# Optimization experiments

Measured on AMD Instinct MI355X. Metric: run time of the kernel, lower is better.

Reference implementation:

```python
import jax, jax.numpy as jnp
import numpy as np

N = 512          # data_info['n']
K = 513          # data_info['k'] + 1
B = 65536        # batch size


def _build_adjust(n, k):
    # Reproduces the __init__ mask construction exactly.
    a1 = np.ones((n - 1, k - 1, 2), dtype=np.float32)
    a2 = np.zeros((n - 1, k - 1, 2), dtype=np.float32)
    for i in range(0, k - 2):
        if i >= n - 1:
            break
        f1 = a1[i].reshape(-1)
        f1[2 + 2 * i:] = 0
        a1[i] = f1.reshape(k - 1, 2)
        f2 = a2[i].reshape(-1)
        f2[2 + 2 * i + 1] = 1
        a2[i] = f2.reshape(k - 1, 2)
    return jnp.asarray(a1), jnp.asarray(a2)


W_ADJ1, W_ADJ2 = _build_adjust(N, K)


def setup_inputs() -> dict:
    key = jax.random.key(0)
    k1, k2, k3 = jax.random.split(key, 3)
    x = jax.random.randint(k1, (B, N), 0, 2, dtype=jnp.int32)
    W = jax.random.normal(k2, (N - 1, K - 1, 2), dtype=jnp.float32)
    endW = jax.random.normal(k3, (1, K), dtype=jnp.float32)
    return {"x": x, "W": W, "endW": endW}


def reference(x, W, endW):
    # W_full construction (softmax over the 2-way split, masked, with the
    # deterministic [1,0] row prepended along the group axis).
    Wsm = jax.nn.softmax(W, axis=2)                      # (n-1, k-1, 2)
    W_full = Wsm * W_ADJ1 + W_ADJ2                       # (n-1, k-1, 2)
    append = jnp.zeros((N - 1, 1, 2), W_full.dtype).at[:, :, 0].set(1.0)
    W_full = jnp.concatenate([append, W_full], axis=1)   # (n-1, k, 2)

    # group_num at step i is the running cumsum of x[:, 0..i]; the serial
    # recurrence collapses to a single cumsum, letting us gather all steps
    # at once instead of the original n-1 step Python loop.
    g = jnp.cumsum(x, axis=1)                            # (B, n)
    steps = jnp.arange(N - 1)                            # step i -> W_full[i-1]
    vals = W_full[steps[None, :], g[:, 1:], x[:, 1:]]    # (B, n-1)
    out = jnp.sum(jnp.log(vals), axis=1, keepdims=True)  # (B, 1)

    e = jax.nn.softmax(endW, axis=1)[0]                  # (k,)
    out = out + jnp.log(e[g[:, -1]])[:, None]            # (B, 1)
    return out
```

## Files before the change

kernel.cpp:

```cpp
#include <hip/hip_runtime.h>
#include <math.h>

#define NN      512
#define KK      513
#define BB      65536
#define TROWS   512
#define TCOLS   513
#define T16STR  528

#define RPB     64
#define NSEG    8
#define SEGW    64
#define BLK     (RPB * NSEG)
#define XSTR    129
#define TPB2    2

typedef int iv4 __attribute__((ext_vector_type(4)));

__device__ __forceinline__ unsigned f2bf(float f) {
    unsigned u = __float_as_uint(f);
    return (u + 0x7fffu + ((u >> 16) & 1u)) >> 16;
}

__global__ void build_table_kernel(const float* __restrict__ W, unsigned* __restrict__ T16) {
    int idx = blockIdx.x * blockDim.x + threadIdx.x;
    if (idx >= TROWS * TCOLS) return;
    int t = idx / TCOLS;
    int g = idx - t * TCOLS;
    float v0 = 0.f, v1 = 0.f;
    if (t >= 1 && g >= 1 && g <= t) {
        const float* w = W + ((size_t)(t - 1) * (KK - 1) + (g - 1)) * 2;
        float w0 = w[0], w1 = w[1];
        float m  = fmaxf(w0, w1);
        float lse = m + logf(expf(w0 - m) + expf(w1 - m));
        v0 = w0 - lse;
        v1 = w1 - lse;
    }
    T16[t * T16STR + g] = f2bf(v0) | (f2bf(v1) << 16);
}

__global__ void build_endw_kernel(const float* __restrict__ endW, float* __restrict__ logE) {
    int lane = threadIdx.x;
    float vals[9];
    float m = -1e30f;
    #pragma unroll
    for (int k = 0; k < 9; ++k) {
        int i = lane + 64 * k;
        vals[k] = (i < KK) ? endW[i] : -1e30f;
        m = fmaxf(m, vals[k]);
    }
    #pragma unroll
    for (int d = 32; d >= 1; d >>= 1) m = fmaxf(m, __shfl_xor(m, d, 64));
    float s = 0.f;
    #pragma unroll
    for (int k = 0; k < 9; ++k) s += expf(vals[k] - m);
    #pragma unroll
    for (int d = 32; d >= 1; d >>= 1) s += __shfl_xor(s, d, 64);
    float lse = m + logf(s);
    #pragma unroll
    for (int k = 0; k < 9; ++k) {
        int i = lane + 64 * k;
        if (i < KK) logE[i] = endW[i] - lse;
    }
}

__global__ __launch_bounds__(BLK, 4) void pc_main_kernel(
    const int* __restrict__ x, const unsigned* __restrict__ T16,
    const float* __restrict__ logE, float* __restrict__ out)
{
    __shared__ unsigned xb[2][RPB * XSTR];
    __shared__ int      segsum[NSEG * RPB];
    __shared__ float    partial[NSEG * RPB];

    const int tid   = threadIdx.x;
    const int seg   = tid >> 6;
    const int lane  = tid & 63;
    const int rowbb = blockIdx.x * (RPB * TPB2);

    {
        const iv4* tile = (const iv4*)(x + (size_t)rowbb * NN);
        #pragma unroll
        for (int j = 0; j < 16; ++j) {
            int i = tid + BLK * j;
            iv4 a = __builtin_nontemporal_load(&tile[i]);
            unsigned m = (unsigned)(a.x & 1) | ((unsigned)(a.y & 1) << 8)
                       | ((unsigned)(a.z & 1) << 16) | ((unsigned)(a.w & 1) << 24);
            xb[0][(i >> 7) * XSTR + (i & 127)] = m;
        }
    }
    __syncthreads();

    int cur = 0;
    iv4 S[16];
    #pragma unroll
    for (int t = 0; t < TPB2; ++t) {
        const int row0 = rowbb + t * RPB;

        if (t + 1 < TPB2) {
            const iv4* tile = (const iv4*)(x + (size_t)(row0 + RPB) * NN);
            #pragma unroll
            for (int j = 0; j < 16; ++j) S[j] = __builtin_nontemporal_load(&tile[tid + BLK * j]);
        }

        unsigned w[16];
        int ssum = 0;
        #pragma unroll
        for (int m = 0; m < 16; ++m) {
            w[m] = xb[cur][lane * XSTR + seg * 16 + m];
            ssum += __popc(w[m]);
        }
        segsum[seg * 64 + lane] = ssum;
        __syncthreads();

        int g = 0, gtot = 0;
        #pragma unroll
        for (int s = 0; s < NSEG; ++s) {
            int v = segsum[s * 64 + lane];
            if (s < seg) g += v;
            gtot += v;
        }

        float a0 = 0.f, a1 = 0.f, a2 = 0.f, a3 = 0.f;
        const unsigned* Tseg = T16 + (size_t)(seg * SEGW) * T16STR;
        #pragma unroll
        for (int m = 0; m < 16; ++m) {
            const unsigned* Tm = Tseg + (size_t)(4 * m) * T16STR;
            unsigned wm = w[m];
            int b0 = wm & 1;         g += b0; unsigned u0 = Tm[0 * T16STR + g];
            a0 += __uint_as_float(b0 ? (u0 & 0xffff0000u) : (u0 << 16));
            int b1 = (wm >> 8)  & 1; g += b1; unsigned u1 = Tm[1 * T16STR + g];
            a1 += __uint_as_float(b1 ? (u1 & 0xffff0000u) : (u1 << 16));
            int b2 = (wm >> 16) & 1; g += b2; unsigned u2 = Tm[2 * T16STR + g];
            a2 += __uint_as_float(b2 ? (u2 & 0xffff0000u) : (u2 << 16));
            int b3 = (wm >> 24) & 1; g += b3; unsigned u3 = Tm[3 * T16STR + g];
            a3 += __uint_as_float(b3 ? (u3 & 0xffff0000u) : (u3 << 16));
        }
        partial[seg * 64 + lane] = (a0 + a1) + (a2 + a3);

        if (t + 1 < TPB2) {
            #pragma unroll
            for (int j = 0; j < 16; ++j) {
                int i = tid + BLK * j;
                unsigned m = (unsigned)(S[j].x & 1) | ((unsigned)(S[j].y & 1) << 8)
                           | ((unsigned)(S[j].z & 1) << 16) | ((unsigned)(S[j].w & 1) << 24);
                xb[cur ^ 1][(i >> 7) * XSTR + (i & 127)] = m;
            }
        }
        __syncthreads();

        if (seg == 0) {
            float s = logE[gtot];
            #pragma unroll
            for (int q = 0; q < NSEG; ++q) s += partial[q * 64 + lane];
            out[row0 + lane] = s;
        }
        cur ^= 1;
    }
}

extern "C" void kernel_launch(void* const* d_in, const int* in_sizes, int n_in,
                              void* d_out, int out_size, void* d_ws, size_t ws_size,
                              hipStream_t stream)
{
    const int*   x    = (const int*)d_in[0];
    const float* W    = (const float*)d_in[1];
    const float* endW = (const float*)d_in[2];
    float*       out  = (float*)d_out;

    unsigned* T16  = (unsigned*)d_ws;
    float*    logE = (float*)((char*)d_ws + (size_t)TROWS * T16STR * sizeof(unsigned));

    {
        int total  = TROWS * TCOLS;
        int blocks = (total + 255) / 256;
        build_table_kernel<<<blocks, 256, 0, stream>>>(W, T16);
    }
    build_endw_kernel<<<1, 64, 0, stream>>>(endW, logE);
    pc_main_kernel<<<BB / (RPB * TPB2), BLK, 0, stream>>>(x, T16, logE, out);
}
```

Measured before the change: 220.8 us.

## Drop in-block double-buffered prefetch, process one tile per block with higher occupancy

The main kernel no longer handles two 64-row tiles per block with register prefetch and a double-buffered LDS. Each block now handles a single tile, so the grid doubles. The launch bound is raised to request 8 blocks per CU instead of 4. The aim is to hide memory latency through occupancy rather than explicit software pipelining, freeing registers and halving LDS use. The cost is more blocks and no overlap of the next load with the table gathers inside a block.

After: 201.7 us. 8.6% less time.

```diff
diff --git a/kernel.cpp b/kernel.cpp
--- a/kernel.cpp
+++ b/kernel.cpp
@@ -13,7 +13,6 @@
 #define SEGW    64
 #define BLK     (RPB * NSEG)
 #define XSTR    129
-#define TPB2    2
 
 typedef int iv4 __attribute__((ext_vector_type(4)));
 
@@ -64,97 +63,74 @@
     }
 }
 
-__global__ __launch_bounds__(BLK, 4) void pc_main_kernel(
+__global__ __launch_bounds__(BLK, 8) void pc_main_kernel(
     const int* __restrict__ x, const unsigned* __restrict__ T16,
     const float* __restrict__ logE, float* __restrict__ out)
 {
-    __shared__ unsigned xb[2][RPB * XSTR];
+    __shared__ unsigned xb[RPB * XSTR];
     __shared__ int      segsum[NSEG * RPB];
     __shared__ float    partial[NSEG * RPB];
 
-    const int tid   = threadIdx.x;
-    const int seg   = tid >> 6;
-    const int lane  = tid & 63;
-    const int rowbb = blockIdx.x * (RPB * TPB2);
+    const int tid  = threadIdx.x;
+    const int row0 = blockIdx.x * RPB;
 
     {
-        const iv4* tile = (const iv4*)(x + (size_t)rowbb * NN);
+        const iv4* tile = (const iv4*)(x + (size_t)row0 * NN);
         #pragma unroll
         for (int j = 0; j < 16; ++j) {
             int i = tid + BLK * j;
             iv4 a = __builtin_nontemporal_load(&tile[i]);
             unsigned m = (unsigned)(a.x & 1) | ((unsigned)(a.y & 1) << 8)
                        | ((unsigned)(a.z & 1) << 16) | ((unsigned)(a.w & 1) << 24);
-            xb[0][(i >> 7) * XSTR + (i & 127)] = m;
+            xb[(i >> 7) * XSTR + (i & 127)] = m;
         }
     }
     __syncthreads();
 
-    int cur = 0;
-    iv4 S[16];
+    const int seg  = tid >> 6;
+    const int lane = tid & 63;
+
+    unsigned w[16];
+    int ssum = 0;
     #pragma unroll
-    for (int t = 0; t < TPB2; ++t) {
-        const int row0 = rowbb + t * RPB;
+    for (int m = 0; m < 16; ++m) {
+        w[m] = xb[lane * XSTR + seg * 16 + m];
+        ssum += __popc(w[m]);
+    }
+    segsum[seg * 64 + lane] = ssum;
+    __syncthreads();
 
-        if (t + 1 < TPB2) {
-            const iv4* tile = (const iv4*)(x + (size_t)(row0 + RPB) * NN);
-            #pragma unroll
-            for (int j = 0; j < 16; ++j) S[j] = __builtin_nontemporal_load(&tile[tid + BLK * j]);
-        }
+    int g = 0, gtot = 0;
+    #pragma unroll
+    for (int s = 0; s < NSEG; ++s) {
+        int v = segsum[s * 64 + lane];
+        if (s < seg) g += v;
+        gtot += v;
+    }
 
-        unsigned w[16];
-        int ssum = 0;
+    float a0 = 0.f, a1 = 0.f, a2 = 0.f, a3 = 0.f;
+    const unsigned* Tseg = T16 + (size_t)(seg * SEGW) * T16STR;
+    #pragma unroll
+    for (int m = 0; m < 16; ++m) {
+        const unsigned* Tm = Tseg + (size_t)(4 * m) * T16STR;
+        unsigned wm = w[m];
+        int b0 = wm & 1;         g += b0; unsigned u0 = Tm[0 * T16STR + g];
+        a0 += __uint_as_float(b0 ? (u0 & 0xffff0000u) : (u0 << 16));
+        int b1 = (wm >> 8)  & 1; g += b1; unsigned u1 = Tm[1 * T16STR + g];
+        a1 += __uint_as_float(b1 ? (u1 & 0xffff0000u) : (u1 << 16));
+        int b2 = (wm >> 16) & 1; g += b2; unsigned u2 = Tm[2 * T16STR + g];
+        a2 += __uint_as_float(b2 ? (u2 & 0xffff0000u) : (u2 << 16));
+        int b3 = (wm >> 24) & 1; g += b3; unsigned u3 = Tm[3 * T16STR + g];
+        a3 += __uint_as_float(b3 ? (u3 & 0xffff0000u) : (u3 << 16));
+    }
+    partial[seg * 64 + lane] = (a0 + a1) + (a2 + a3);
+    __syncthreads();
+
+    if (seg == 0) {
+        float s = logE[gtot];
         #pragma unroll
-        for (int m = 0; m < 16; ++m) {
-            w[m] = xb[cur][lane * XSTR + seg * 16 + m];
-            ssum += __popc(w[m]);
-        }
-        segsum[seg * 64 + lane] = ssum;
-        __syncthreads();
-
-        int g = 0, gtot = 0;
-        #pragma unroll
-        for (int s = 0; s < NSEG; ++s) {
-            int v = segsum[s * 64 + lane];
-            if (s < seg) g += v;
-            gtot += v;
-        }
-
-        float a0 = 0.f, a1 = 0.f, a2 = 0.f, a3 = 0.f;
-        const unsigned* Tseg = T16 + (size_t)(seg * SEGW) * T16STR;
-        #pragma unroll
-        for (int m = 0; m < 16; ++m) {
-            const unsigned* Tm = Tseg + (size_t)(4 * m) * T16STR;
-            unsigned wm = w[m];
-            int b0 = wm & 1;         g += b0; unsigned u0 = Tm[0 * T16STR + g];
-            a0 += __uint_as_float(b0 ? (u0 & 0xffff0000u) : (u0 << 16));
-            int b1 = (wm >> 8)  & 1; g += b1; unsigned u1 = Tm[1 * T16STR + g];
-            a1 += __uint_as_float(b1 ? (u1 & 0xffff0000u) : (u1 << 16));
-            int b2 = (wm >> 16) & 1; g += b2; unsigned u2 = Tm[2 * T16STR + g];
-            a2 += __uint_as_float(b2 ? (u2 & 0xffff0000u) : (u2 << 16));
-            int b3 = (wm >> 24) & 1; g += b3; unsigned u3 = Tm[3 * T16STR + g];
-            a3 += __uint_as_float(b3 ? (u3 & 0xffff0000u) : (u3 << 16));
-        }
-        partial[seg * 64 + lane] = (a0 + a1) + (a2 + a3);
-
-        if (t + 1 < TPB2) {
-            #pragma unroll
-            for (int j = 0; j < 16; ++j) {
-                int i = tid + BLK * j;
-                unsigned m = (unsigned)(S[j].x & 1) | ((unsigned)(S[j].y & 1) << 8)
-                           | ((unsigned)(S[j].z & 1) << 16) | ((unsigned)(S[j].w & 1) << 24);
-                xb[cur ^ 1][(i >> 7) * XSTR + (i & 127)] = m;
-            }
-        }
-        __syncthreads();
-
-        if (seg == 0) {
-            float s = logE[gtot];
-            #pragma unroll
-            for (int q = 0; q < NSEG; ++q) s += partial[q * 64 + lane];
-            out[row0 + lane] = s;
-        }
-        cur ^= 1;
+        for (int t = 0; t < NSEG; ++t) s += partial[t * 64 + lane];
+        out[row0 + lane] = s;
     }
 }
 
@@ -176,5 +152,5 @@
         build_table_kernel<<<blocks, 256, 0, stream>>>(W, T16);
     }
     build_endw_kernel<<<1, 64, 0, stream>>>(endW, logE);
-    pc_main_kernel<<<BB / (RPB * TPB2), BLK, 0, stream>>>(x, T16, logE, out);
+    pc_main_kernel<<<BB / RPB, BLK, 0, stream>>>(x, T16, logE, out);
 }
```
